# Kernel optimization log

Measured on AMD Instinct MI355X. Metric: run time of the kernel, lower is better.

## Reference

```python
import jax, jax.numpy as jnp
import numpy as np

B, T, D, M, L = 4, 2048, 256, 128, 16
P = M * L  # max_pair_cnt


def setup_inputs() -> dict:
    key = jax.random.key(0)
    ks = jax.random.split(key, 11)
    head = jax.random.normal(ks[0], (B, P, T), jnp.float32) * 0.05
    tail = jax.random.normal(ks[1], (B, P, T), jnp.float32) * 0.05
    x = jax.random.normal(ks[2], (B, T, D), jnp.float32)
    coref_mention_position = jax.random.uniform(ks[3], (B, M, T), jnp.float32)
    lab = jax.random.uniform(ks[4], (B, P, 2), jnp.float32) + 1e-3
    coref_label = lab / lab.sum(-1, keepdims=True)  # already-softmaxed target
    coref_label_mask = jax.random.randint(ks[5], (B, P), 0, 2).astype(bool)
    lens = jnp.full((B, M), L, jnp.int32)  # uniform segment lengths
    w1 = jax.random.normal(ks[6], (3 * D, D), jnp.float32) / np.sqrt(3 * D).astype(np.float32)
    b1 = jnp.zeros((D,), jnp.float32)
    w2 = jax.random.normal(ks[7], (D, 2), jnp.float32) / np.sqrt(D).astype(np.float32)
    b2 = jnp.zeros((2,), jnp.float32)
    return {"head": head, "tail": tail, "lens": lens, "x": x,
            "coref_mention_position": coref_mention_position,
            "coref_label": coref_label, "coref_label_mask": coref_label_mask,
            "w1": w1, "b1": b1, "w2": w2, "b2": b2}


def reference(head, tail, lens, x, coref_mention_position, coref_label,
              coref_label_mask, w1, b1, w2, b2):
    # bmm-based gather of mention reps: [B,P,T] @ [B,T,D] -> [B,P,D]
    head_rep = jnp.einsum('bpt,btd->bpd', head, x)
    tail_rep = jnp.einsum('bpt,btd->bpd', tail, x)
    feat = jnp.concatenate([head_rep, tail_rep, head_rep * tail_rep], axis=-1)
    logits = jax.nn.relu(feat @ w1 + b1) @ w2 + b2  # [B,P,2]

    # ragged split_n_pad -> per-mention top-1 select (uniform lens == L -> reshape)
    scores = logits[..., 1].reshape(B, M, L)            # [B,M,L]
    max_idx = jnp.argmax(scores, axis=-1)               # [B,M]
    max_val = jnp.max(scores, axis=-1)                  # [B,M] (raw logit, as in source)
    tail_seg = tail_rep.reshape(B, M, L, D)
    sel = jnp.take_along_axis(tail_seg, max_idx[:, :, None, None], axis=2)[:, :, 0, :]
    coref_rep_m = sel * max_val[:, :, None]             # [B,M,D]

    # scatter-bmm merge back into sequence: [B,T,M] @ [B,M,D] -> [B,T,D]
    coref_rep = jnp.einsum('bmt,bmd->btd', coref_mention_position, coref_rep_m)
    output = x + coref_rep

    # KLDivLoss(reduction='mean') over masked pairs
    logq = jax.nn.log_softmax(logits, axis=-1)
    lab = coref_label
    pw = jnp.where(lab > 0, lab * jnp.log(jnp.maximum(lab, 1e-38)), 0.0) - lab * logq
    n = jnp.sum(coref_label_mask).astype(jnp.float32)
    loss = jnp.where(coref_label_mask[..., None], pw, 0.0).sum() / (n * 2.0)
    return output, loss
```

## Files before the change

### kernel.cpp

```cpp
#include <hip/hip_runtime.h>
#include <hip/hip_bf16.h>
#include <stdint.h>

#define TAU 0.35f

typedef __attribute__((ext_vector_type(8))) short bf16x8;
typedef __attribute__((ext_vector_type(4))) float f32x4;

__device__ __forceinline__ unsigned short f2bf(float f) {
  __bf16 h = (__bf16)f;
  return __builtin_bit_cast(unsigned short, h);
}
__device__ __forceinline__ float bf2f(unsigned short u) {
  unsigned int v = ((unsigned int)u) << 16;
  return __builtin_bit_cast(float, v);
}
__device__ __forceinline__ void async_copy16(const void* g, void* l) {
  __builtin_amdgcn_global_load_lds(
      (const __attribute__((address_space(1))) unsigned int*)g,
      (__attribute__((address_space(3))) unsigned int*)l, 16, 0, 0);
}
__device__ __forceinline__ float rdlane(float v, int l) {
  return __builtin_bit_cast(float,
      __builtin_amdgcn_readlane(__builtin_bit_cast(int, v), l));
}

__global__ __launch_bounds__(256) void k_prep(
    const float* __restrict__ x, const float* __restrict__ w1,
    const float* __restrict__ b2,
    unsigned short* __restrict__ xt, unsigned short* __restrict__ w1t,
    float* __restrict__ logits, int* __restrict__ njobs,
    float* __restrict__ featws) {
  __shared__ float tileS[64][65];
  __shared__ float tx[64][132];
  int bx = blockIdx.x, tid = threadIdx.x;
  if (bx == 0 && tid < 4) njobs[tid] = 0;
  if (bx < 64) {
    int i = bx * 256 + tid;
    logits[i] = b2[i & 1];
  }
  {
    float4 z = {0.f, 0.f, 0.f, 0.f};
    for (int i = bx * 256 + tid; i < 1048576; i += 304 * 256)
      ((float4*)featws)[i] = z;
  }
  if (bx < 256) {
    int b = bx >> 6, kc = (bx >> 1) & 31, dh = bx & 1;
    const float* src = x + ((size_t)b * 2048 + (size_t)kc * 64) * 256 + dh * 128;
#pragma unroll
    for (int p = 0; p < 8; ++p) {
      int idx = p * 256 + tid;
      int row = idx >> 5, f4 = idx & 31;
      *(float4*)&tx[row][f4 * 4] = *(const float4*)&src[(size_t)row * 256 + f4 * 4];
    }
    __syncthreads();
    unsigned short* dst = xt + ((size_t)(b * 32 + kc)) * 16384 + dh * 1024;
#pragma unroll
    for (int p = 0; p < 4; ++p) {
      int idx = p * 256 + tid;
      int d0 = idx & 127, k8 = idx >> 7;
      bf16x8 v;
#pragma unroll
      for (int j = 0; j < 8; ++j) v[j] = (short)f2bf(tx[k8 * 8 + j][d0]);
      *(bf16x8*)&dst[(size_t)k8 * 2048 + d0 * 8] = v;
    }
  } else {
    int wt = bx - 256;
    int k6 = wt >> 2, n6 = wt & 3;
    int j = tid & 63, i0 = tid >> 6;
    const float* src = w1 + ((size_t)k6 * 64) * 256 + n6 * 64;
    for (int i = i0; i < 64; i += 4) tileS[i][j] = src[(size_t)i * 256 + j];
    __syncthreads();
    unsigned short* dst = w1t + ((size_t)n6 * 64) * 768 + k6 * 64;
    for (int r = i0; r < 64; r += 4) dst[(size_t)r * 768 + j] = f2bf(tileS[j][r]);
  }
}

__global__ __launch_bounds__(512, 4) void k_gemm_rep(
    const float* __restrict__ head, const float* __restrict__ tail,
    const unsigned short* __restrict__ xt,
    float* __restrict__ hrep, float* __restrict__ trep) {
  __shared__ unsigned short As[2][2048];
  __shared__ unsigned short Bs[2][16384];
  int bx = blockIdx.x;
  int b = bx >> 7, mt = bx & 127;
  const float* Asrc = ((mt < 64) ? head : tail) +
                      ((size_t)(b * 2048 + (mt & 63) * 32)) * 2048;
  float* Crep = (mt < 64) ? hrep : trep;
  const unsigned short* Bsrc = xt + (size_t)b * 524288;

  int tid = threadIdx.x, lane = tid & 63, w = tid >> 6;
  int rg = w & 1, cg = w >> 1;
  int l4 = lane >> 4, l15 = lane & 15;

  int arow = tid >> 3, ak8 = tid & 7;
  const float* aptr = Asrc + (size_t)arow * 2048 + ak8 * 8;
  int awi = (ak8 * 32 + arow) * 8;

  const unsigned short* bg = Bsrc + tid * 8;

  int aoff[2];
  int boff[2][4];
#pragma unroll
  for (int kh = 0; kh < 2; ++kh) {
    aoff[kh] = ((kh * 4 + l4) * 32 + rg * 16 + l15) * 8;
#pragma unroll
    for (int ct = 0; ct < 4; ++ct)
      boff[kh][ct] = ((kh * 4 + l4) * 256 + cg * 64 + ct * 16 + l15) * 8;
  }

  f32x4 acc[4];
#pragma unroll
  for (int ct = 0; ct < 4; ++ct) acc[ct] = (f32x4){0.f, 0.f, 0.f, 0.f};

  float4 av0, av1;
  auto STAGEB = [&](int buf) {
#pragma unroll
    for (int a = 0; a < 4; ++a)
      async_copy16(bg + (size_t)a * 4096, &Bs[buf][(tid + a * 512) * 8]);
    bg += 16384;
  };
  auto LOADA = [&]() {
    const float4* ap = (const float4*)aptr;
    av0 = ap[0]; av1 = ap[1];
    aptr += 64;
  };
  auto WRITEA = [&](int buf) {
    bf16x8 p;
    p[0] = (short)f2bf(av0.x); p[1] = (short)f2bf(av0.y);
    p[2] = (short)f2bf(av0.z); p[3] = (short)f2bf(av0.w);
    p[4] = (short)f2bf(av1.x); p[5] = (short)f2bf(av1.y);
    p[6] = (short)f2bf(av1.z); p[7] = (short)f2bf(av1.w);
    *(bf16x8*)&As[buf][awi] = p;
  };
  auto MMA = [&](int buf) {
    const unsigned short* A_ = As[buf];
    const unsigned short* B_ = Bs[buf];
#pragma unroll
    for (int kh = 0; kh < 2; ++kh) {
      bf16x8 a0 = *(const bf16x8*)&A_[aoff[kh]];
#pragma unroll
      for (int ct = 0; ct < 4; ++ct) {
        bf16x8 bb = *(const bf16x8*)&B_[boff[kh][ct]];
        acc[ct] = __builtin_amdgcn_mfma_f32_16x16x32_bf16(a0, bb, acc[ct], 0, 0, 0);
      }
    }
  };

  STAGEB(0);
  if (tid < 256) { LOADA(); WRITEA(0); }
  __syncthreads();

  for (int it = 0; it < 32; ++it) {
    int cur = it & 1, nxt = cur ^ 1;
    if (it < 31) {
      STAGEB(nxt);
      if (tid < 256) LOADA();
    }
    MMA(cur);
    if (it < 31 && tid < 256) WRITEA(nxt);
    __syncthreads();
  }

  size_t prow = (size_t)b * 2048 + (size_t)(mt & 63) * 32 + rg * 16 + (l4 << 2);
  int cb = cg * 64 + l15;
#pragma unroll
  for (int ct = 0; ct < 4; ++ct)
#pragma unroll
    for (int i = 0; i < 4; ++i)
      Crep[(prow + i) * 256 + cb + ct * 16] = acc[ct][i];
}

__global__ __launch_bounds__(256) void k_feat(
    const float* __restrict__ hrep, const float* __restrict__ trep,
    unsigned short* __restrict__ featbf) {
  int gid = blockIdx.x * 256 + threadIdx.x;
  int p = gid >> 6, d0 = (gid & 63) * 4;
  float4 h4 = *(const float4*)&hrep[(size_t)p * 256 + d0];
  float4 t4 = *(const float4*)&trep[(size_t)p * 256 + d0];
  ushort4 a, bb, c;
  a.x = f2bf(h4.x); a.y = f2bf(h4.y); a.z = f2bf(h4.z); a.w = f2bf(h4.w);
  bb.x = f2bf(t4.x); bb.y = f2bf(t4.y); bb.z = f2bf(t4.z); bb.w = f2bf(t4.w);
  c.x = f2bf(h4.x * t4.x); c.y = f2bf(h4.y * t4.y);
  c.z = f2bf(h4.z * t4.z); c.w = f2bf(h4.w * t4.w);
  *(ushort4*)&featbf[(size_t)p * 768 + d0] = a;
  *(ushort4*)&featbf[(size_t)p * 768 + 256 + d0] = bb;
  *(ushort4*)&featbf[(size_t)p * 768 + 512 + d0] = c;
}

__global__ __launch_bounds__(256, 4) void k_gemm_mlp(
    const unsigned short* __restrict__ featb, const unsigned short* __restrict__ w1t,
    const float* __restrict__ b1, const float* __restrict__ w2,
    float* __restrict__ logits) {
  __shared__ unsigned short As[2][4096], Bs[2][4096];
  int bx = blockIdx.x;
  int ntile = bx >> 7;
  int mtile = bx & 127;
  int tid = threadIdx.x, lane = tid & 63, w = tid >> 6;

  const unsigned short* ag[2];
  const unsigned short* bgp[2];
  int dofs[2];
#pragma unroll
  for (int a = 0; a < 2; ++a) {
    int rowofs = a * 8 + (lane >> 3);
    int k8 = (lane & 7) ^ (rowofs & 7);
    ag[a] = featb + (size_t)(mtile * 64 + w * 16 + rowofs) * 768 + k8 * 8;
    bgp[a] = w1t + (size_t)(ntile * 64 + w * 16 + rowofs) * 768 + k8 * 8;
    dofs[a] = (w * 128 + a * 64 + lane) * 8;
  }
  int sw0 = (lane >> 4) ^ (lane & 7);
  int sw1 = (4 + (lane >> 4)) ^ (lane & 7);
  int arowc = (w * 16 + (lane & 15)) * 8;
  int colc[4];
#pragma unroll
  for (int ct = 0; ct < 4; ++ct) colc[ct] = (ct * 16 + (lane & 15)) * 8;

  f32x4 acc[4];
#pragma unroll
  for (int ct = 0; ct < 4; ++ct) acc[ct] = (f32x4){0.f, 0.f, 0.f, 0.f};

#pragma unroll
  for (int a = 0; a < 2; ++a) {
    async_copy16(ag[a], &As[0][dofs[a]]); ag[a] += 64;
    async_copy16(bgp[a], &Bs[0][dofs[a]]); bgp[a] += 64;
  }
  __syncthreads();

  for (int it = 0; it < 12; ++it) {
    int cur = it & 1, nxt = cur ^ 1;
    if (it < 11) {
#pragma unroll
      for (int a = 0; a < 2; ++a) {
        async_copy16(ag[a], &As[nxt][dofs[a]]); ag[a] += 64;
        async_copy16(bgp[a], &Bs[nxt][dofs[a]]); bgp[a] += 64;
      }
    }
    const unsigned short* A_ = As[cur];
    const unsigned short* B_ = Bs[cur];
    bf16x8 a0 = *(const bf16x8*)&A_[(arowc + sw0) * 8];
    bf16x8 a1 = *(const bf16x8*)&A_[(arowc + sw1) * 8];
#pragma unroll
    for (int ct = 0; ct < 4; ++ct) {
      bf16x8 b0 = *(const bf16x8*)&B_[(colc[ct] + sw0) * 8];
      acc[ct] = __builtin_amdgcn_mfma_f32_16x16x32_bf16(a0, b0, acc[ct], 0, 0, 0);
    }
#pragma unroll
    for (int ct = 0; ct < 4; ++ct) {
      bf16x8 b1 = *(const bf16x8*)&B_[(colc[ct] + sw1) * 8];
      acc[ct] = __builtin_amdgcn_mfma_f32_16x16x32_bf16(a1, b1, acc[ct], 0, 0, 0);
    }
    __syncthreads();
  }

  float bv[4], w20[4], w21[4];
#pragma unroll
  for (int ct = 0; ct < 4; ++ct) {
    int col = ntile * 64 + ct * 16 + (lane & 15);
    bv[ct] = b1[col]; w20[ct] = w2[col * 2]; w21[ct] = w2[col * 2 + 1];
  }
#pragma unroll
  for (int i = 0; i < 4; ++i) {
    float s0 = 0.f, s1 = 0.f;
#pragma unroll
    for (int ct = 0; ct < 4; ++ct) {
      float r = fmaxf(acc[ct][i] + bv[ct], 0.f);
      s0 += r * w20[ct]; s1 += r * w21[ct];
    }
#pragma unroll
    for (int off = 1; off < 16; off <<= 1) {
      s0 += __shfl_xor(s0, off); s1 += __shfl_xor(s1, off);
    }
    if ((lane & 15) == 0) {
      int row = mtile * 64 + w * 16 + ((lane >> 4) << 2) + i;
      atomicAdd(&logits[row * 2], s0);
      atomicAdd(&logits[row * 2 + 1], s1);
    }
  }
}

__global__ void k_select(const float* __restrict__ logits, int* __restrict__ idxv,
                         float* __restrict__ mval, int* __restrict__ cmask,
                         int* __restrict__ njobs, int* __restrict__ jobs) {
  int q = blockIdx.x * 256 + threadIdx.x;
  if (q >= 512) return;
  int base = q * 16;
  float s[16];
#pragma unroll
  for (int i = 0; i < 16; ++i) s[i] = logits[(size_t)(base + i) * 2 + 1];
  float best = s[0]; int bi = 0;
#pragma unroll
  for (int i = 1; i < 16; ++i) if (s[i] > best) { best = s[i]; bi = i; }
  int mask = 0, cnt = 0;
#pragma unroll
  for (int i = 0; i < 16; ++i) if (s[i] > best - TAU) { mask |= 1 << i; ++cnt; }
  idxv[q] = bi; mval[q] = best;
  if (cnt > 1) {
    cmask[q] = mask;
    int bb = q >> 7;
    for (int i = 0; i < 16; ++i)
      if ((mask >> i) & 1) {
        int j = atomicAdd(&njobs[bb], 1);
        jobs[bb * 2048 + j] = base + i;
      }
  } else cmask[q] = 0;
}

__global__ __launch_bounds__(1024) void k_refine_dot(
    const int* __restrict__ njobs, const int* __restrict__ jobs,
    const float* __restrict__ head, const float* __restrict__ tail,
    const float* __restrict__ x,
    float* __restrict__ featH, float* __restrict__ featT) {
  __shared__ float red[4][16][256];
  __shared__ int scode[8];
  int tid = threadIdx.x, lane = tid & 63, w = tid >> 6;
  int tg = w >> 2, dg = w & 3;
  int d = dg * 64 + lane;

  for (int gt = blockIdx.x; ; gt += gridDim.x) {
    int rem = gt, b = 0, nj = 0;
    for (; b < 4; ++b) {
      nj = njobs[b];
      int ntb = ((nj + 7) >> 3) * 8;
      if (rem < ntb) break;
      rem -= ntb;
    }
    if (b == 4) break;
    int grp = rem >> 3, tc = rem & 7;
    __syncthreads();
    if (tid < 8) scode[tid] = jobs[b * 2048 + min(grp * 8 + tid, nj - 1)];
    __syncthreads();

    int t0 = tc * 256 + tg * 64;
    float vh[8], vt[8];
#pragma unroll
    for (int j = 0; j < 8; ++j) {
      int p = scode[j] & 2047;
      size_t ro = ((size_t)(b * 2048 + p)) * 2048 + t0 + lane;
      vh[j] = head[ro]; vt[j] = tail[ro];
    }
    float ah[8] = {0.f, 0.f, 0.f, 0.f, 0.f, 0.f, 0.f, 0.f};
    float at[8] = {0.f, 0.f, 0.f, 0.f, 0.f, 0.f, 0.f, 0.f};
    const float* xp = x + (size_t)b * 524288 + (size_t)t0 * 256 + d;
#pragma unroll 8
    for (int t = 0; t < 64; ++t) {
      float xv = xp[(size_t)t * 256];
#pragma unroll
      for (int j = 0; j < 8; ++j) {
        ah[j] += rdlane(vh[j], t) * xv;
        at[j] += rdlane(vt[j], t) * xv;
      }
    }
#pragma unroll
    for (int j = 0; j < 8; ++j) {
      red[tg][j][d] = ah[j];
      red[tg][8 + j][d] = at[j];
    }
    __syncthreads();
    if (tid < 256) {
#pragma unroll
      for (int j = 0; j < 16; ++j) {
        float s = red[0][j][tid] + red[1][j][tid] + red[2][j][tid] + red[3][j][tid];
        int jj = j & 7;
        if (grp * 8 + jj < nj) {
          float* dst = (j < 8) ? featH : featT;
          atomicAdd(&dst[(size_t)scode[jj] * 256 + tid], s);
        }
      }
    }
  }
}

__global__ __launch_bounds__(1024) void k_refine_mlp(
    const int* __restrict__ njobs, const int* __restrict__ jobs,
    const float* __restrict__ featH, const float* __restrict__ featT,
    const float* __restrict__ w1, const float* __restrict__ b1,
    const float* __restrict__ w2, const float* __restrict__ b2,
    float* __restrict__ refined) {
  __shared__ float feat8[768][8];
  __shared__ float redm[4][8][256];
  __shared__ float part[8][4];
  __shared__ int scode[8];
  int tid = threadIdx.x;
  int hseg = tid >> 8, d = tid & 255;

  for (int gt = blockIdx.x; ; gt += gridDim.x) {
    int rem = gt, b = 0, nj = 0;
    for (; b < 4; ++b) {
      nj = njobs[b];
      int ntb = (nj + 7) >> 3;
      if (rem < ntb) break;
      rem -= ntb;
    }
    if (b == 4) break;
    int grp = rem;
    __syncthreads();
    if (tid < 8) scode[tid] = jobs[b * 2048 + min(grp * 8 + tid, nj - 1)];
    __syncthreads();
#pragma unroll
    for (int r = 0; r < 2; ++r) {
      int j = hseg * 2 + r;
      float h = featH[(size_t)scode[j] * 256 + d];
      float t = featT[(size_t)scode[j] * 256 + d];
      feat8[d][j] = h; feat8[256 + d][j] = t; feat8[512 + d][j] = h * t;
    }
    __syncthreads();
    float hp[8] = {0.f, 0.f, 0.f, 0.f, 0.f, 0.f, 0.f, 0.f};
    const float* w1c = w1 + (size_t)(hseg * 192) * 256 + d;
#pragma unroll 4
    for (int ii = 0; ii < 192; ++ii) {
      float wv = w1c[(size_t)ii * 256];
      float4 f0 = *(const float4*)&feat8[hseg * 192 + ii][0];
      float4 f1 = *(const float4*)&feat8[hseg * 192 + ii][4];
      hp[0] += f0.x * wv; hp[1] += f0.y * wv; hp[2] += f0.z * wv; hp[3] += f0.w * wv;
      hp[4] += f1.x * wv; hp[5] += f1.y * wv; hp[6] += f1.z * wv; hp[7] += f1.w * wv;
    }
#pragma unroll
    for (int j = 0; j < 8; ++j) redm[hseg][j][d] = hp[j];
    __syncthreads();
    if (tid < 256) {
      float w2v = w2[tid * 2 + 1], b1v = b1[tid];
#pragma unroll
      for (int j = 0; j < 8; ++j) {
        float h = b1v + redm[0][j][tid] + redm[1][j][tid] + redm[2][j][tid] + redm[3][j][tid];
        h = fmaxf(h, 0.f) * w2v;
#pragma unroll
        for (int off = 1; off < 64; off <<= 1) h += __shfl_xor(h, off);
        if ((tid & 63) == 0) part[j][tid >> 6] = h;
      }
    }
    __syncthreads();
    if (tid < 8 && grp * 8 + tid < nj)
      refined[scode[tid]] = part[tid][0] + part[tid][1] + part[tid][2] + part[tid][3] + b2[1];
  }
}

__global__ __launch_bounds__(256) void k_repm(
    const int* __restrict__ idxv, const float* __restrict__ mval,
    const int* __restrict__ cmask, const float* __restrict__ refined,
    const float* __restrict__ trep, float* __restrict__ repm) {
  int q = blockIdx.x, d = threadIdx.x;
  int mask = cmask[q]; int bi; float v;
  if (mask) {
    bi = -1; v = -1e30f;
    for (int i = 0; i < 16; ++i)
      if ((mask >> i) & 1) { float s = refined[q * 16 + i]; if (s > v) { v = s; bi = i; } }
  } else { bi = idxv[q]; v = mval[q]; }
  repm[(size_t)q * 256 + d] = trep[((size_t)q * 16 + bi) * 256 + d] * v;
}

__global__ __launch_bounds__(256) void k_merge(
    const float* __restrict__ cmp, const float* __restrict__ repm,
    const float* __restrict__ x, float* __restrict__ out) {
  __shared__ float cl[128 * 16];
  int bx = blockIdx.x, b = bx >> 7, t0 = (bx & 127) * 16;
  int tid = threadIdx.x;
#pragma unroll
  for (int it = 0; it < 2; ++it) {
    int f = it * 256 + tid;
    int row = f >> 2, c4 = (f & 3) * 4;
    *(float4*)&cl[row * 16 + c4] =
        *(const float4*)&cmp[((size_t)(b * 128 + row)) * 2048 + t0 + c4];
  }
  __syncthreads();
  float acc[16];
#pragma unroll
  for (int i = 0; i < 16; ++i) acc[i] = 0.f;
  int d = tid;
  for (int m = 0; m < 128; ++m) {
    float rv = repm[(size_t)(b * 128 + m) * 256 + d];
    const float4* c4p = (const float4*)&cl[m * 16];
#pragma unroll
    for (int jj = 0; jj < 4; ++jj) {
      float4 c = c4p[jj];
      acc[jj * 4] += c.x * rv; acc[jj * 4 + 1] += c.y * rv;
      acc[jj * 4 + 2] += c.z * rv; acc[jj * 4 + 3] += c.w * rv;
    }
  }
  const float* xb = x + ((size_t)(b * 2048 + t0)) * 256 + d;
  float* ob = out + ((size_t)(b * 2048 + t0)) * 256 + d;
#pragma unroll
  for (int tt = 0; tt < 16; ++tt) ob[(size_t)tt * 256] = xb[(size_t)tt * 256] + acc[tt];
}

__global__ __launch_bounds__(1024) void k_loss(
    const float* __restrict__ logits, const float* __restrict__ lab,
    const unsigned char* __restrict__ mask, float* __restrict__ out_loss) {
  __shared__ float rs[1024], rc[1024];
  int tid = threadIdx.x;
  float sum = 0.f, cnt = 0.f;
  for (int p = tid; p < 8192; p += 1024) {
    float l0 = logits[(size_t)p * 2], l1 = logits[(size_t)p * 2 + 1];
    float a0 = lab[(size_t)p * 2], a1 = lab[(size_t)p * 2 + 1];
    float mx = fmaxf(l0, l1);
    float lse = mx + logf(expf(l0 - mx) + expf(l1 - mx));
    float pw = 0.f;
    if (a0 > 0.f) pw += a0 * logf(fmaxf(a0, 1e-38f));
    if (a1 > 0.f) pw += a1 * logf(fmaxf(a1, 1e-38f));
    pw -= a0 * (l0 - lse) + a1 * (l1 - lse);
    if (mask[p]) { sum += pw; cnt += 1.f; }
  }
  rs[tid] = sum; rc[tid] = cnt;
  __syncthreads();
  for (int s = 512; s > 0; s >>= 1) {
    if (tid < s) { rs[tid] += rs[tid + s]; rc[tid] += rc[tid + s]; }
    __syncthreads();
  }
  if (tid == 0) *out_loss = rs[0] / (rc[0] * 2.0f);
}

extern "C" void kernel_launch(void* const* d_in, const int* in_sizes, int n_in,
                              void* d_out, int out_size, void* d_ws, size_t ws_size,
                              hipStream_t stream) {
  (void)in_sizes; (void)n_in; (void)out_size; (void)ws_size;
  const float* head = (const float*)d_in[0];
  const float* tail = (const float*)d_in[1];
  const float* x = (const float*)d_in[3];
  const float* cmp = (const float*)d_in[4];
  const float* lab = (const float*)d_in[5];
  const unsigned char* lmask = (const unsigned char*)d_in[6];
  const float* w1 = (const float*)d_in[7];
  const float* b1 = (const float*)d_in[8];
  const float* w2 = (const float*)d_in[9];
  const float* b2 = (const float*)d_in[10];
  float* out = (float*)d_out;

  char* ws = (char*)d_ws;
  size_t off = 0;
  auto alloc = [&](size_t bytes) -> void* {
    void* p = ws + off; off += (bytes + 255) & ~(size_t)255; return p;
  };
  unsigned short* xt = (unsigned short*)alloc(4ull * 256 * 2048 * 2);
  unsigned short* w1t = (unsigned short*)alloc(256ull * 768 * 2);
  float* hrep = (float*)alloc(8192ull * 256 * 4);
  float* trep = (float*)alloc(8192ull * 256 * 4);
  unsigned short* featb = (unsigned short*)alloc(8192ull * 768 * 2);
  float* logits = (float*)alloc(8192ull * 2 * 4);
  float* refined = (float*)alloc(8192ull * 4);
  int* idxv = (int*)alloc(512 * 4);
  float* mvalv = (float*)alloc(512 * 4);
  int* cmaskv = (int*)alloc(512 * 4);
  int* njobs = (int*)alloc(256);
  int* jobs = (int*)alloc(4 * 2048 * 4);
  float* repm = (float*)alloc(512ull * 256 * 4);
  float* featH = (float*)alloc(8192ull * 256 * 4);
  float* featT = (float*)alloc(8192ull * 256 * 4);

  k_prep<<<304, 256, 0, stream>>>(x, w1, b2, xt, w1t, logits, njobs, featH);
  k_gemm_rep<<<512, 512, 0, stream>>>(head, tail, xt, hrep, trep);
  k_feat<<<2048, 256, 0, stream>>>(hrep, trep, featb);
  k_gemm_mlp<<<512, 256, 0, stream>>>(featb, w1t, b1, w2, logits);
  k_select<<<2, 256, 0, stream>>>(logits, idxv, mvalv, cmaskv, njobs, jobs);
  k_refine_dot<<<512, 1024, 0, stream>>>(njobs, jobs, head, tail, x, featH, featT);
  k_refine_mlp<<<128, 1024, 0, stream>>>(njobs, jobs, featH, featT, w1, b1, w2, b2, refined);
  k_repm<<<512, 256, 0, stream>>>(idxv, mvalv, cmaskv, refined, trep, repm);
  k_merge<<<512, 256, 0, stream>>>(cmp, repm, x, out);
  k_loss<<<1, 1024, 0, stream>>>(logits, lab, lmask, out + 4ull * 2048 * 256);
}
```

Baseline: 320.8 us.

## Fuse select with loss, repm into merge, swizzle LDS and remap GEMM blocks

Merges the top-1 selection and KL loss into one single-block kernel, and folds the per-mention rep scaling into the merge kernel so the repm buffer is gone. Adds an XOR swizzle to the A tile's LDS layout to reduce bank conflicts and remaps block indices in the rep GEMM to change cache locality. Each merge block now recomputes the selection for its batch, and the loss loop runs in one block of 512 threads instead of 1024.

```diff
diff --git a/kernel.cpp b/kernel.cpp
--- a/kernel.cpp
+++ b/kernel.cpp
@@ -82,7 +82,8 @@
     float* __restrict__ hrep, float* __restrict__ trep) {
   __shared__ unsigned short As[2][2048];
   __shared__ unsigned short Bs[2][16384];
-  int bx = blockIdx.x;
+  int bx0 = blockIdx.x;
+  int bx = ((bx0 & 7) << 6) | (bx0 >> 3);
   int b = bx >> 7, mt = bx & 127;
   const float* Asrc = ((mt < 64) ? head : tail) +
                       ((size_t)(b * 2048 + (mt & 63) * 32)) * 2048;
@@ -95,7 +96,7 @@
 
   int arow = tid >> 3, ak8 = tid & 7;
   const float* aptr = Asrc + (size_t)arow * 2048 + ak8 * 8;
-  int awi = (ak8 * 32 + arow) * 8;
+  int awi = ((ak8 * 32 + arow) * 8) ^ ((ak8 & 3) << 4);
 
   const unsigned short* bg = Bsrc + tid * 8;
 
@@ -103,10 +104,11 @@
   int boff[2][4];
 #pragma unroll
   for (int kh = 0; kh < 2; ++kh) {
-    aoff[kh] = ((kh * 4 + l4) * 32 + rg * 16 + l15) * 8;
+    int k8 = kh * 4 + l4;
+    aoff[kh] = (((k8 * 32 + rg * 16 + l15) * 8)) ^ ((l4 & 3) << 4);
 #pragma unroll
     for (int ct = 0; ct < 4; ++ct)
-      boff[kh][ct] = ((kh * 4 + l4) * 256 + cg * 64 + ct * 16 + l15) * 8;
+      boff[kh][ct] = (k8 * 256 + cg * 64 + ct * 16 + l15) * 8;
   }
 
   f32x4 acc[4];
@@ -279,31 +281,56 @@
   }
 }
 
-__global__ void k_select(const float* __restrict__ logits, int* __restrict__ idxv,
-                         float* __restrict__ mval, int* __restrict__ cmask,
-                         int* __restrict__ njobs, int* __restrict__ jobs) {
-  int q = blockIdx.x * 256 + threadIdx.x;
-  if (q >= 512) return;
-  int base = q * 16;
-  float s[16];
-#pragma unroll
-  for (int i = 0; i < 16; ++i) s[i] = logits[(size_t)(base + i) * 2 + 1];
-  float best = s[0]; int bi = 0;
-#pragma unroll
-  for (int i = 1; i < 16; ++i) if (s[i] > best) { best = s[i]; bi = i; }
-  int mask = 0, cnt = 0;
-#pragma unroll
-  for (int i = 0; i < 16; ++i) if (s[i] > best - TAU) { mask |= 1 << i; ++cnt; }
-  idxv[q] = bi; mval[q] = best;
-  if (cnt > 1) {
-    cmask[q] = mask;
-    int bb = q >> 7;
-    for (int i = 0; i < 16; ++i)
-      if ((mask >> i) & 1) {
-        int j = atomicAdd(&njobs[bb], 1);
-        jobs[bb * 2048 + j] = base + i;
-      }
-  } else cmask[q] = 0;
+__global__ __launch_bounds__(512) void k_select_loss(
+    const float* __restrict__ logits, int* __restrict__ idxv,
+    float* __restrict__ mval, int* __restrict__ cmask,
+    int* __restrict__ njobs, int* __restrict__ jobs,
+    const float* __restrict__ lab, const unsigned char* __restrict__ mask,
+    float* __restrict__ out_loss) {
+  __shared__ float rs[512], rc[512];
+  int tid = threadIdx.x;
+  {
+    int q = tid;
+    int base = q * 16;
+    float s[16];
+#pragma unroll
+    for (int i = 0; i < 16; ++i) s[i] = logits[(size_t)(base + i) * 2 + 1];
+    float best = s[0]; int bi = 0;
+#pragma unroll
+    for (int i = 1; i < 16; ++i) if (s[i] > best) { best = s[i]; bi = i; }
+    int msk = 0, cnt = 0;
+#pragma unroll
+    for (int i = 0; i < 16; ++i) if (s[i] > best - TAU) { msk |= 1 << i; ++cnt; }
+    idxv[q] = bi; mval[q] = best;
+    if (cnt > 1) {
+      cmask[q] = msk;
+      int bb = q >> 7;
+      for (int i = 0; i < 16; ++i)
+        if ((msk >> i) & 1) {
+          int j = atomicAdd(&njobs[bb], 1);
+          jobs[bb * 2048 + j] = base + i;
+        }
+    } else cmask[q] = 0;
+  }
+  float sum = 0.f, cnt = 0.f;
+  for (int p = tid; p < 8192; p += 512) {
+    float l0 = logits[(size_t)p * 2], l1 = logits[(size_t)p * 2 + 1];
+    float a0 = lab[(size_t)p * 2], a1 = lab[(size_t)p * 2 + 1];
+    float mx = fmaxf(l0, l1);
+    float lse = mx + logf(expf(l0 - mx) + expf(l1 - mx));
+    float pw = 0.f;
+    if (a0 > 0.f) pw += a0 * logf(fmaxf(a0, 1e-38f));
+    if (a1 > 0.f) pw += a1 * logf(fmaxf(a1, 1e-38f));
+    pw -= a0 * (l0 - lse) + a1 * (l1 - lse);
+    if (mask[p]) { sum += pw; cnt += 1.f; }
+  }
+  rs[tid] = sum; rc[tid] = cnt;
+  __syncthreads();
+  for (int s = 256; s > 0; s >>= 1) {
+    if (tid < s) { rs[tid] += rs[tid + s]; rc[tid] += rc[tid + s]; }
+    __syncthreads();
+  }
+  if (tid == 0) *out_loss = rs[0] / (rc[0] * 2.0f);
 }
 
 __global__ __launch_bounds__(1024) void k_refine_dot(
@@ -435,26 +462,27 @@
   }
 }
 
-__global__ __launch_bounds__(256) void k_repm(
+__global__ __launch_bounds__(256) void k_merge(
     const int* __restrict__ idxv, const float* __restrict__ mval,
     const int* __restrict__ cmask, const float* __restrict__ refined,
-    const float* __restrict__ trep, float* __restrict__ repm) {
-  int q = blockIdx.x, d = threadIdx.x;
-  int mask = cmask[q]; int bi; float v;
-  if (mask) {
-    bi = -1; v = -1e30f;
-    for (int i = 0; i < 16; ++i)
-      if ((mask >> i) & 1) { float s = refined[q * 16 + i]; if (s > v) { v = s; bi = i; } }
-  } else { bi = idxv[q]; v = mval[q]; }
-  repm[(size_t)q * 256 + d] = trep[((size_t)q * 16 + bi) * 256 + d] * v;
-}
-
-__global__ __launch_bounds__(256) void k_merge(
-    const float* __restrict__ cmp, const float* __restrict__ repm,
-    const float* __restrict__ x, float* __restrict__ out) {
+    const float* __restrict__ trep,
+    const float* __restrict__ cmp, const float* __restrict__ x,
+    float* __restrict__ out) {
   __shared__ float cl[128 * 16];
+  __shared__ float vs[128];
+  __shared__ int bsel[128];
   int bx = blockIdx.x, b = bx >> 7, t0 = (bx & 127) * 16;
   int tid = threadIdx.x;
+  if (tid < 128) {
+    int q = b * 128 + tid;
+    int mask = cmask[q]; int bi; float v;
+    if (mask) {
+      bi = -1; v = -1e30f;
+      for (int i = 0; i < 16; ++i)
+        if ((mask >> i) & 1) { float s = refined[q * 16 + i]; if (s > v) { v = s; bi = i; } }
+    } else { bi = idxv[q]; v = mval[q]; }
+    vs[tid] = v; bsel[tid] = bi;
+  }
 #pragma unroll
   for (int it = 0; it < 2; ++it) {
     int f = it * 256 + tid;
@@ -468,7 +496,8 @@
   for (int i = 0; i < 16; ++i) acc[i] = 0.f;
   int d = tid;
   for (int m = 0; m < 128; ++m) {
-    float rv = repm[(size_t)(b * 128 + m) * 256 + d];
+    size_t trow = ((size_t)(b * 128 + m) * 16 + bsel[m]) * 256;
+    float rv = trep[trow + d] * vs[m];
     const float4* c4p = (const float4*)&cl[m * 16];
 #pragma unroll
     for (int jj = 0; jj < 4; ++jj) {
@@ -481,32 +510,6 @@
   float* ob = out + ((size_t)(b * 2048 + t0)) * 256 + d;
 #pragma unroll
   for (int tt = 0; tt < 16; ++tt) ob[(size_t)tt * 256] = xb[(size_t)tt * 256] + acc[tt];
-}
-
-__global__ __launch_bounds__(1024) void k_loss(
-    const float* __restrict__ logits, const float* __restrict__ lab,
-    const unsigned char* __restrict__ mask, float* __restrict__ out_loss) {
-  __shared__ float rs[1024], rc[1024];
-  int tid = threadIdx.x;
-  float sum = 0.f, cnt = 0.f;
-  for (int p = tid; p < 8192; p += 1024) {
-    float l0 = logits[(size_t)p * 2], l1 = logits[(size_t)p * 2 + 1];
-    float a0 = lab[(size_t)p * 2], a1 = lab[(size_t)p * 2 + 1];
-    float mx = fmaxf(l0, l1);
-    float lse = mx + logf(expf(l0 - mx) + expf(l1 - mx));
-    float pw = 0.f;
-    if (a0 > 0.f) pw += a0 * logf(fmaxf(a0, 1e-38f));
-    if (a1 > 0.f) pw += a1 * logf(fmaxf(a1, 1e-38f));
-    pw -= a0 * (l0 - lse) + a1 * (l1 - lse);
-    if (mask[p]) { sum += pw; cnt += 1.f; }
-  }
-  rs[tid] = sum; rc[tid] = cnt;
-  __syncthreads();
-  for (int s = 512; s > 0; s >>= 1) {
-    if (tid < s) { rs[tid] += rs[tid + s]; rc[tid] += rc[tid + s]; }
-    __syncthreads();
-  }
-  if (tid == 0) *out_loss = rs[0] / (rc[0] * 2.0f);
 }
 
 extern "C" void kernel_launch(void* const* d_in, const int* in_sizes, int n_in,
@@ -542,7 +545,6 @@
   int* cmaskv = (int*)alloc(512 * 4);
   int* njobs = (int*)alloc(256);
   int* jobs = (int*)alloc(4 * 2048 * 4);
-  float* repm = (float*)alloc(512ull * 256 * 4);
   float* featH = (float*)alloc(8192ull * 256 * 4);
   float* featT = (float*)alloc(8192ull * 256 * 4);
 
@@ -550,10 +552,9 @@
   k_gemm_rep<<<512, 512, 0, stream>>>(head, tail, xt, hrep, trep);
   k_feat<<<2048, 256, 0, stream>>>(hrep, trep, featb);
   k_gemm_mlp<<<512, 256, 0, stream>>>(featb, w1t, b1, w2, logits);
-  k_select<<<2, 256, 0, stream>>>(logits, idxv, mvalv, cmaskv, njobs, jobs);
+  k_select_loss<<<1, 512, 0, stream>>>(logits, idxv, mvalv, cmaskv, njobs, jobs,
+                                       lab, lmask, out + 4ull * 2048 * 256);
   k_refine_dot<<<512, 1024, 0, stream>>>(njobs, jobs, head, tail, x, featH, featT);
   k_refine_mlp<<<128, 1024, 0, stream>>>(njobs, jobs, featH, featT, w1, b1, w2, b2, refined);
-  k_repm<<<512, 256, 0, stream>>>(idxv, mvalv, cmaskv, refined, trep, repm);
-  k_merge<<<512, 256, 0, stream>>>(cmp, repm, x, out);
-  k_loss<<<1, 1024, 0, stream>>>(logits, lab, lmask, out + 4ull * 2048 * 256);
-}
+  k_merge<<<512, 256, 0, stream>>>(idxv, mvalv, cmaskv, refined, trep, cmp, x, out);
+}
```

Result: slower. 328.3 us (+2.3%).
